# Optimization experiments

Measured on AMD Instinct MI355X. Metric: run time of the kernel, lower is better.

Reference implementation:

```python
import jax, jax.numpy as jnp
import numpy as np

B, S, E, D = 256, 256, 2, 128  # batch, seq_len, encoder_dim, decoder_dim


def setup_inputs() -> dict:
    key = jax.random.key(0)
    ks = jax.random.split(key, 9)
    u = lambda k, shape, n: jax.random.uniform(k, shape, jnp.float32, -1.0 / np.sqrt(n), 1.0 / np.sqrt(n))
    return {
        "out_encoder": jax.random.normal(ks[0], (B, S, E), jnp.float32),
        "W1_w": u(ks[1], (S, S), S),            # Linear(seq_len, seq_len)
        "W1_b": u(ks[2], (S,), S),
        "W2_w": u(ks[3], (S, 2 * S), 2 * S),    # Linear(2*seq_len, seq_len)
        "W2_b": u(ks[4], (S,), 2 * S),
        "W_ih": u(ks[5], (4 * D, E), D),        # LSTMCell input weights (i,f,g,o)
        "W_hh": u(ks[6], (4 * D, D), D),
        "b_ih": u(ks[7], (4 * D,), D),
        "b_hh": u(ks[8], (4 * D,), D),
    }


def reference(out_encoder, W1_w, W1_b, W2_w, W2_b, W_ih, W_hh, b_ih, b_hh):
    b, s, e = out_encoder.shape
    d = W_hh.shape[1]
    dt = out_encoder.dtype

    # W_2 term: encoder flattened to [B, 2S]; identical every step, hoist it.
    w2term = out_encoder.reshape(b, s * e) @ W2_w.T + W2_b          # [B, S]
    # W_1 applied to a row of S copies of h_d equals h_d * rowsum(W1) + b.
    w1sum = W1_w.sum(axis=1)                                        # [S]

    def attn(h):  # h: [B, D] -> context [B, E]
        hterm = h[:, :, None] * w1sum[None, None, :] + W1_b         # [B, D, S]
        en = jnp.tanh(w2term[:, None, :] + hterm)                   # [B, D, S]
        alpha = jax.nn.softmax(en, axis=-1).mean(axis=1)            # [B, S] (softmax over seq)
        return jnp.einsum('bs,bse->be', alpha, out_encoder)         # [B, E]

    def lstm_cell(x, h, c):
        gates = x @ W_ih.T + h @ W_hh.T + b_ih + b_hh               # [B, 4D]
        i, f, g, o = jnp.split(gates, 4, axis=-1)
        c = jax.nn.sigmoid(f) * c + jax.nn.sigmoid(i) * jnp.tanh(g)
        h = jax.nn.sigmoid(o) * jnp.tanh(c)
        return h, c

    h0 = jnp.zeros((b, d), dt)
    c0 = jnp.zeros((b, d), dt)

    def step(carry, _):
        h, c = carry
        x = attn(h)
        h, c = lstm_cell(x, h, c)
        return (h, c), h

    _, hs = jax.lax.scan(step, (h0, c0), None, length=s)
    return hs  # [S, B, D]: stacked decoder hidden states (original returns a list of h_t)
```

## Files before the change

### kernel.cpp

```cpp
#include <hip/hip_runtime.h>

#define NB 256
#define NS 256
#define NE 2
#define ND 128
#define NT 512
#define NN 16
#define RING 32
#define SLOT 144
#define SLOTH 160

typedef float vf4 __attribute__((ext_vector_type(4)));
typedef _Float16 f16x2 __attribute__((ext_vector_type(2)));

constexpr float L2E = 1.4426950408889634f;
constexpr float PI_F = 3.14159265358979323846f;

__device__ const float CT[16][16] = {
 {1,0,0,0,0,0,0,0,0,0,0,0,0,0,0,0},
 {0,1,0,0,0,0,0,0,0,0,0,0,0,0,0,0},
 {-1,0,2,0,0,0,0,0,0,0,0,0,0,0,0,0},
 {0,-3,0,4,0,0,0,0,0,0,0,0,0,0,0,0},
 {1,0,-8,0,8,0,0,0,0,0,0,0,0,0,0,0},
 {0,5,0,-20,0,16,0,0,0,0,0,0,0,0,0,0},
 {-1,0,18,0,-48,0,32,0,0,0,0,0,0,0,0,0},
 {0,-7,0,56,0,-112,0,64,0,0,0,0,0,0,0,0},
 {1,0,-32,0,160,0,-256,0,128,0,0,0,0,0,0,0},
 {0,9,0,-120,0,432,0,-576,0,256,0,0,0,0,0,0},
 {-1,0,50,0,-400,0,1120,0,-1280,0,512,0,0,0,0,0},
 {0,-11,0,220,0,-1232,0,2816,0,-2816,0,1024,0,0,0,0},
 {1,0,-72,0,840,0,-3584,0,6912,0,-6144,0,2048,0,0,0},
 {0,13,0,-364,0,2912,0,-9984,0,16640,0,-13312,0,4096,0,0},
 {-1,0,98,0,-1568,0,9408,0,-26880,0,39424,0,-28672,0,8192,0},
 {0,-15,0,560,0,-6048,0,28800,0,-70400,0,92160,0,-61440,0,16384}};

template <int C>
__device__ __forceinline__ float dppadd(float x) {
    return x + __builtin_bit_cast(float,
        __builtin_amdgcn_update_dpp(0, __builtin_bit_cast(int, x), C, 0xF, 0xF, true));
}
__device__ __forceinline__ float red_quad(float x) {
    x = dppadd<0xB1>(x); x = dppadd<0x4E>(x); return x;
}
__device__ __forceinline__ float red_oct(float x) {
    x = dppadd<0xB1>(x); x = dppadd<0x4E>(x); x = dppadd<0x141>(x); return x;
}
__device__ __forceinline__ float red_wave64(float x) {
    x = dppadd<0xB1>(x); x = dppadd<0x4E>(x); x = dppadd<0x141>(x);
    x = dppadd<0x140>(x); x = dppadd<0x142>(x); x = dppadd<0x143>(x); return x;
}
__device__ __forceinline__ float red_half32(float x) {
    x = dppadd<0xB1>(x); x = dppadd<0x4E>(x); x = dppadd<0x141>(x);
    x = dppadd<0x140>(x); x = dppadd<0x142>(x); return x;
}
__device__ __forceinline__ float red_grp16(float x) {
    x = dppadd<0x141>(x); x = dppadd<0x140>(x);
    x = dppadd<0x142>(x); x = dppadd<0x143>(x); return x;
}

__global__ __launch_bounds__(NT, 2)
void attn_lstm_decoder(const float* __restrict__ enc,
                       const float* __restrict__ W1w,
                       const float* __restrict__ W1b,
                       const float* __restrict__ W2w,
                       const float* __restrict__ W2b,
                       const float* __restrict__ Wih,
                       const float* __restrict__ Whh,
                       const float* __restrict__ bih,
                       const float* __restrict__ bhh,
                       float* __restrict__ out)
{
    const int b    = blockIdx.x;
    const int t    = threadIdx.x;
    const int wave = t >> 6;
    const int lane = t & 63;
    const int g    = t >> 2;
    const int q    = t & 3;
    const bool qb0 = q & 1;
    const bool qb1 = q & 2;
    const int half = lane >> 5;
    const int idx  = lane & 31;
    const int jnode = 2 * wave + half;

    __shared__ __align__(16) float    hist[RING * SLOT];
    __shared__ __align__(16) _Float16 hist16[RING * SLOTH];
    __shared__ __align__(16) float xwbuf[2][16];
    __shared__ float A2_l[NS];
    __shared__ float g2_l[NS];
    __shared__ float e0_l[NS];
    __shared__ float e1_l[NS];
    __shared__ float Ml[NN * NN];
    __shared__ float2 Pn[NN];
    __shared__ float2 Vl[NN];
    __shared__ float Pm0[NN], Pm1[NN];

    {
        float v = enc[b * (NS * NE) + t];
        if (t & 1) e1_l[t >> 1] = v; else e0_l[t >> 1] = v;
    }
    if (t < NN * NN) {
        const int mi = t >> 4, mj = t & 15;
        const float w = (mi == 0) ? (1.0f / NN) : (2.0f / NN);
        Ml[t] = w * __cosf((float)(mi * (2 * mj + 1)) * (PI_F / (2 * NN)));
    }
    __syncthreads();

    for (int r = 0; r < 32; ++r) {
        const int s = wave * 32 + r;
        float p = W1w[s * NS + lane]       + W1w[s * NS + lane + 64]
                + W1w[s * NS + lane + 128] + W1w[s * NS + lane + 192];
        p = red_wave64(p);
        if (lane == 63) g2_l[s] = p * (2.0f * L2E);
        float qq = 0.0f;
        #pragma unroll
        for (int kk = 0; kk < 8; ++kk) {
            const int c = lane + kk * 64;
            const float ev = (c & 1) ? e1_l[c >> 1] : e0_l[c >> 1];
            qq = fmaf(ev, W2w[s * (2 * NS) + c], qq);
        }
        qq = red_wave64(qq);
        if (lane == 63) A2_l[s] = (qq + W2b[s] + W1b[s]) * (2.0f * L2E);
    }
    __syncthreads();

    {
        const float y  = __cosf((float)(2 * jnode + 1) * (PI_F / (2 * NN)));
        const float C2 = -2.0f * L2E;
        float l = 0.0f, p0 = 0.0f, p1 = 0.0f;
        #pragma unroll
        for (int k = 0; k < 8; ++k) {
            const int s = k * 32 + idx;
            const float m1 = fmaf(y, g2_l[s], A2_l[s]);
            const float u  = __builtin_amdgcn_exp2f(m1);
            const float rc = __builtin_amdgcn_rcpf(u + 1.0f);
            const float e  = __builtin_amdgcn_exp2f(rc * C2);
            l += e;
            p0 = fmaf(e, e0_l[s], p0);
            p1 = fmaf(e, e1_l[s], p1);
        }
        l = red_half32(l); p0 = red_half32(p0); p1 = red_half32(p1);
        if ((lane & 31) == 31) {
            const float rl = __builtin_amdgcn_rcpf(l);
            Pn[jnode] = make_float2(p0 * rl, p1 * rl);
        }
    }
    __syncthreads();

    if (t < NN) {
        float v0 = 0.0f, v1 = 0.0f;
        #pragma unroll
        for (int j = 0; j < NN; ++j) {
            v0 = fmaf(Ml[t * NN + j], Pn[j].x, v0);
            v1 = fmaf(Ml[t * NN + j], Pn[j].y, v1);
        }
        Vl[t] = make_float2(v0 * (1.0f / ND), v1 * (1.0f / ND));
    }

    f16x2 wr16[4][16];
    float wi0_[4], wi1_[4], bb_[4];
    #pragma unroll
    for (int j = 0; j < 4; ++j) {
        const int r = g + 128 * j;
        const vf4* W4 = reinterpret_cast<const vf4*>(Whh + r * ND + q * 32);
        #pragma unroll
        for (int i = 0; i < 8; ++i) {
            const vf4 w = W4[i];
            wr16[j][2 * i + 0] = f16x2{(_Float16)w.x, (_Float16)w.y};
            wr16[j][2 * i + 1] = f16x2{(_Float16)w.z, (_Float16)w.w};
        }
        wi0_[j] = Wih[r * 2 + 0];
        wi1_[j] = Wih[r * 2 + 1];
        bb_[j]  = bih[r] + bhh[r];
    }

    if (t < ND) {
        hist[31 * SLOT + 36 * (t >> 5) + (t & 31)] = 0.0f;
        hist16[31 * SLOTH + 40 * (t >> 5) + (t & 31)] = (_Float16)0.0f;
    }
    float h_reg = 0.0f, c_reg = 0.0f;
    __syncthreads();

    if (t < NN) {
        float s0 = 0.0f, s1 = 0.0f;
        #pragma unroll
        for (int k = 0; k < NN; ++k) {
            s0 = fmaf(Vl[k].x, CT[k][t], s0);
            s1 = fmaf(Vl[k].y, CT[k][t], s1);
        }
        Pm0[t] = s0; Pm1[t] = s1;
    }
    __syncthreads();

    float Q0[4], Q1[4];
    #pragma unroll
    for (int i = 0; i < 4; ++i) { Q0[i] = Pm0[4 * i + q]; Q1[i] = Pm1[4 * i + q]; }

    auto phaseG = [&](float h, int pw) {
        const float h2 = h * h;
        const float h3 = h2 * h;
        const float h4 = h2 * h2;
        const float hq = qb1 ? (qb0 ? h3 : h2) : (qb0 ? h : 1.0f);
        float a0 = fmaf(Q0[3], h4, Q0[2]);
        a0 = fmaf(a0, h4, Q0[1]);
        a0 = fmaf(a0, h4, Q0[0]);
        float a1 = fmaf(Q1[3], h4, Q1[2]);
        a1 = fmaf(a1, h4, Q1[1]);
        a1 = fmaf(a1, h4, Q1[0]);
        a0 *= hq;
        a1 *= hq;
        a0 = red_quad(a0);  a1 = red_quad(a1);
        a0 = red_grp16(a0); a1 = red_grp16(a1);
        if (lane == 63) {
            xwbuf[pw][2 * wave + 0] = a0;
            xwbuf[pw][2 * wave + 1] = a1;
        }
    };

    phaseG(0.0f, 0);
    __syncthreads();

    for (int step = 0; step < NS; ++step) {
        const int pr = step & 1;
        const int rs = (step + RING - 1) & (RING - 1);
        const int ws = step & (RING - 1);

        float2 xv = *reinterpret_cast<const float2*>(&xwbuf[pr][2 * (lane & 7)]);
        const int4* hb = reinterpret_cast<const int4*>(&hist16[rs * SLOTH + q * 40]);
        int hw[16];
        #pragma unroll
        for (int i = 0; i < 4; ++i) {
            const int4 v = hb[i];
            hw[4 * i + 0] = v.x; hw[4 * i + 1] = v.y;
            hw[4 * i + 2] = v.z; hw[4 * i + 3] = v.w;
        }

        if ((step & 15) == 0 && step > 0) {
            const int sb  = (step - 16) & (RING - 1);
            const int k   = t >> 5;
            const int l32 = t & 31;
            const int w   = 4 * l32;
            const vf4 v = *reinterpret_cast<const vf4*>(
                &hist[(sb + k) * SLOT + 36 * (w >> 5) + (w & 31)]);
            *reinterpret_cast<vf4*>(
                &out[(size_t)(step - 16 + k) * (NB * ND) + b * ND + w]) = v;
        }

        float x0 = red_oct(xv.x);
        float x1 = red_oct(xv.y);

        float d0a = 0.f, d0b = 0.f, d1a = 0.f, d1b = 0.f;
        float d2a = 0.f, d2b = 0.f, d3a = 0.f, d3b = 0.f;
        #pragma unroll
        for (int i = 0; i < 8; ++i) {
            const f16x2 ha = __builtin_bit_cast(f16x2, hw[2 * i + 0]);
            const f16x2 hbv = __builtin_bit_cast(f16x2, hw[2 * i + 1]);
            d0a = __builtin_amdgcn_fdot2(wr16[0][2 * i + 0], ha,  d0a, false);
            d0b = __builtin_amdgcn_fdot2(wr16[0][2 * i + 1], hbv, d0b, false);
            d1a = __builtin_amdgcn_fdot2(wr16[1][2 * i + 0], ha,  d1a, false);
            d1b = __builtin_amdgcn_fdot2(wr16[1][2 * i + 1], hbv, d1b, false);
            d2a = __builtin_amdgcn_fdot2(wr16[2][2 * i + 0], ha,  d2a, false);
            d2b = __builtin_amdgcn_fdot2(wr16[2][2 * i + 1], hbv, d2b, false);
            d3a = __builtin_amdgcn_fdot2(wr16[3][2 * i + 0], ha,  d3a, false);
            d3b = __builtin_amdgcn_fdot2(wr16[3][2 * i + 1], hbv, d3b, false);
        }
        float d0 = d0a + d0b, d1 = d1a + d1b;
        float d2 = d2a + d2b, d3 = d3a + d3b;
        d0 = red_quad(d0);  d1 = red_quad(d1);
        d2 = red_quad(d2);  d3 = red_quad(d3);

        const float gi = d0 + fmaf(x0, wi0_[0], fmaf(x1, wi1_[0], bb_[0]));
        const float gf = d1 + fmaf(x0, wi0_[1], fmaf(x1, wi1_[1], bb_[1]));
        const float gg = d2 + fmaf(x0, wi0_[2], fmaf(x1, wi1_[2], bb_[2]));
        const float go = d3 + fmaf(x0, wi0_[3], fmaf(x1, wi1_[3], bb_[3]));

        const float si = __builtin_amdgcn_rcpf(1.0f + __builtin_amdgcn_exp2f(-L2E * gi));
        const float sf = __builtin_amdgcn_rcpf(1.0f + __builtin_amdgcn_exp2f(-L2E * gf));
        const float so = __builtin_amdgcn_rcpf(1.0f + __builtin_amdgcn_exp2f(-L2E * go));
        const float tg = 1.0f - 2.0f * __builtin_amdgcn_rcpf(__builtin_amdgcn_exp2f(2.0f * L2E * gg) + 1.0f);
        c_reg = sf * c_reg + si * tg;
        const float tc2 = 1.0f - 2.0f * __builtin_amdgcn_rcpf(__builtin_amdgcn_exp2f(2.0f * L2E * c_reg) + 1.0f);
        h_reg = so * tc2;

        if (q == 0) {
            hist[ws * SLOT + 36 * (g >> 5) + (g & 31)] = h_reg;
            hist16[ws * SLOTH + 40 * (g >> 5) + (g & 31)] = (_Float16)h_reg;
        }
        phaseG(h_reg, pr ^ 1);

        __syncthreads();
    }

    {
        const int k   = t >> 5;
        const int l32 = t & 31;
        const int w   = 4 * l32;
        const vf4 v = *reinterpret_cast<const vf4*>(
            &hist[(16 + k) * SLOT + 36 * (w >> 5) + (w & 31)]);
        *reinterpret_cast<vf4*>(
            &out[(size_t)(240 + k) * (NB * ND) + b * ND + w]) = v;
    }
}

extern "C" void kernel_launch(void* const* d_in, const int* in_sizes, int n_in,
                              void* d_out, int out_size, void* d_ws, size_t ws_size,
                              hipStream_t stream) {
    const float* enc = (const float*)d_in[0];
    const float* W1w = (const float*)d_in[1];
    const float* W1b = (const float*)d_in[2];
    const float* W2w = (const float*)d_in[3];
    const float* W2b = (const float*)d_in[4];
    const float* Wih = (const float*)d_in[5];
    const float* Whh = (const float*)d_in[6];
    const float* bih = (const float*)d_in[7];
    const float* bhh = (const float*)d_in[8];
    attn_lstm_decoder<<<NB, NT, 0, stream>>>(enc, W1w, W1b, W2w, W2b,
                                             Wih, Whh, bih, bhh, (float*)d_out);
}
```

Baseline: 303.7 us.

## Compute recurrent h·W_hh gates with MFMA instead of per-thread fdot2

Replaces the per-thread packed fp16 dot products for the recurrent gate matvec with 16x16x32 f16 MFMA tiles, where each wave owns 64 gate rows and the h vector is broadcast as the A operand. Only column 0 of each MFMA result is used. It is written to a new shared gate buffer and read back after an extra block barrier per step. This trades the shuffle reductions and the fdot2 chain for matrix-core work that is mostly wasted (15 of 16 columns), plus one more __syncthreads and an LDS round trip on the serial critical path.

```diff
diff --git a/kernel.cpp b/kernel.cpp
--- a/kernel.cpp
+++ b/kernel.cpp
@@ -11,7 +11,8 @@
 #define SLOTH 160
 
 typedef float vf4 __attribute__((ext_vector_type(4)));
-typedef _Float16 f16x2 __attribute__((ext_vector_type(2)));
+typedef _Float16 f16x8 __attribute__((ext_vector_type(8)));
+typedef float f32x4 __attribute__((ext_vector_type(4)));
 
 constexpr float L2E = 1.4426950408889634f;
 constexpr float PI_F = 3.14159265358979323846f;
@@ -78,6 +79,8 @@
     const int q    = t & 3;
     const bool qb0 = q & 1;
     const bool qb1 = q & 2;
+    const int grp  = lane >> 4;
+    const int nib  = lane & 15;
     const int half = lane >> 5;
     const int idx  = lane & 31;
     const int jnode = 2 * wave + half;
@@ -85,6 +88,7 @@
     __shared__ __align__(16) float    hist[RING * SLOT];
     __shared__ __align__(16) _Float16 hist16[RING * SLOTH];
     __shared__ __align__(16) float xwbuf[2][16];
+    __shared__ __align__(16) float gbuf[4 * ND];
     __shared__ float A2_l[NS];
     __shared__ float g2_l[NS];
     __shared__ float e0_l[NS];
@@ -156,18 +160,26 @@
         Vl[t] = make_float2(v0 * (1.0f / ND), v1 * (1.0f / ND));
     }
 
-    f16x2 wr16[4][16];
+    f16x8 wf[4][4];
     float wi0_[4], wi1_[4], bb_[4];
+    #pragma unroll
+    for (int rt = 0; rt < 4; ++rt) {
+        const int row = 64 * wave + 16 * rt + nib;
+        #pragma unroll
+        for (int kt = 0; kt < 4; ++kt) {
+            const vf4 wa = *reinterpret_cast<const vf4*>(Whh + row * ND + 32 * kt + 8 * grp);
+            const vf4 wb = *reinterpret_cast<const vf4*>(Whh + row * ND + 32 * kt + 8 * grp + 4);
+            f16x8 wv;
+            wv[0] = (_Float16)wa.x; wv[1] = (_Float16)wa.y;
+            wv[2] = (_Float16)wa.z; wv[3] = (_Float16)wa.w;
+            wv[4] = (_Float16)wb.x; wv[5] = (_Float16)wb.y;
+            wv[6] = (_Float16)wb.z; wv[7] = (_Float16)wb.w;
+            wf[rt][kt] = wv;
+        }
+    }
     #pragma unroll
     for (int j = 0; j < 4; ++j) {
         const int r = g + 128 * j;
-        const vf4* W4 = reinterpret_cast<const vf4*>(Whh + r * ND + q * 32);
-        #pragma unroll
-        for (int i = 0; i < 8; ++i) {
-            const vf4 w = W4[i];
-            wr16[j][2 * i + 0] = f16x2{(_Float16)w.x, (_Float16)w.y};
-            wr16[j][2 * i + 1] = f16x2{(_Float16)w.z, (_Float16)w.w};
-        }
         wi0_[j] = Wih[r * 2 + 0];
         wi1_[j] = Wih[r * 2 + 1];
         bb_[j]  = bih[r] + bhh[r];
@@ -224,15 +236,33 @@
         const int rs = (step + RING - 1) & (RING - 1);
         const int ws = step & (RING - 1);
 
+        f16x8 af[4];
+        const _Float16* hsl = &hist16[rs * SLOTH + 8 * grp];
+        #pragma unroll
+        for (int kt = 0; kt < 4; ++kt)
+            af[kt] = __builtin_bit_cast(f16x8,
+                *reinterpret_cast<const int4*>(hsl + 40 * kt));
+
+        f32x4 acc[4];
+        #pragma unroll
+        for (int rt = 0; rt < 4; ++rt) {
+            f32x4 a = {0.0f, 0.0f, 0.0f, 0.0f};
+            #pragma unroll
+            for (int kt = 0; kt < 4; ++kt)
+                a = __builtin_amdgcn_mfma_f32_16x16x32_f16(af[kt], wf[rt][kt], a, 0, 0, 0);
+            acc[rt] = a;
+        }
+        if (lane < 16) {
+            #pragma unroll
+            for (int rt = 0; rt < 4; ++rt) {
+                const int r = 64 * wave + 16 * rt + lane;
+                gbuf[((r & 127) << 2) | (r >> 7)] = acc[rt][0];
+            }
+        }
+        __syncthreads();
+
         float2 xv = *reinterpret_cast<const float2*>(&xwbuf[pr][2 * (lane & 7)]);
-        const int4* hb = reinterpret_cast<const int4*>(&hist16[rs * SLOTH + q * 40]);
-        int hw[16];
-        #pragma unroll
-        for (int i = 0; i < 4; ++i) {
-            const int4 v = hb[i];
-            hw[4 * i + 0] = v.x; hw[4 * i + 1] = v.y;
-            hw[4 * i + 2] = v.z; hw[4 * i + 3] = v.w;
-        }
+        const f32x4 gv = *reinterpret_cast<const f32x4*>(&gbuf[g << 2]);
 
         if ((step & 15) == 0 && step > 0) {
             const int sb  = (step - 16) & (RING - 1);
@@ -248,30 +278,10 @@
         float x0 = red_oct(xv.x);
         float x1 = red_oct(xv.y);
 
-        float d0a = 0.f, d0b = 0.f, d1a = 0.f, d1b = 0.f;
-        float d2a = 0.f, d2b = 0.f, d3a = 0.f, d3b = 0.f;
-        #pragma unroll
-        for (int i = 0; i < 8; ++i) {
-            const f16x2 ha = __builtin_bit_cast(f16x2, hw[2 * i + 0]);
-            const f16x2 hbv = __builtin_bit_cast(f16x2, hw[2 * i + 1]);
-            d0a = __builtin_amdgcn_fdot2(wr16[0][2 * i + 0], ha,  d0a, false);
-            d0b = __builtin_amdgcn_fdot2(wr16[0][2 * i + 1], hbv, d0b, false);
-            d1a = __builtin_amdgcn_fdot2(wr16[1][2 * i + 0], ha,  d1a, false);
-            d1b = __builtin_amdgcn_fdot2(wr16[1][2 * i + 1], hbv, d1b, false);
-            d2a = __builtin_amdgcn_fdot2(wr16[2][2 * i + 0], ha,  d2a, false);
-            d2b = __builtin_amdgcn_fdot2(wr16[2][2 * i + 1], hbv, d2b, false);
-            d3a = __builtin_amdgcn_fdot2(wr16[3][2 * i + 0], ha,  d3a, false);
-            d3b = __builtin_amdgcn_fdot2(wr16[3][2 * i + 1], hbv, d3b, false);
-        }
-        float d0 = d0a + d0b, d1 = d1a + d1b;
-        float d2 = d2a + d2b, d3 = d3a + d3b;
-        d0 = red_quad(d0);  d1 = red_quad(d1);
-        d2 = red_quad(d2);  d3 = red_quad(d3);
-
-        const float gi = d0 + fmaf(x0, wi0_[0], fmaf(x1, wi1_[0], bb_[0]));
-        const float gf = d1 + fmaf(x0, wi0_[1], fmaf(x1, wi1_[1], bb_[1]));
-        const float gg = d2 + fmaf(x0, wi0_[2], fmaf(x1, wi1_[2], bb_[2]));
-        const float go = d3 + fmaf(x0, wi0_[3], fmaf(x1, wi1_[3], bb_[3]));
+        const float gi = gv[0] + fmaf(x0, wi0_[0], fmaf(x1, wi1_[0], bb_[0]));
+        const float gf = gv[1] + fmaf(x0, wi0_[1], fmaf(x1, wi1_[1], bb_[1]));
+        const float gg = gv[2] + fmaf(x0, wi0_[2], fmaf(x1, wi1_[2], bb_[2]));
+        const float go = gv[3] + fmaf(x0, wi0_[3], fmaf(x1, wi1_[3], bb_[3]));
 
         const float si = __builtin_amdgcn_rcpf(1.0f + __builtin_amdgcn_exp2f(-L2E * gi));
         const float sf = __builtin_amdgcn_rcpf(1.0f + __builtin_amdgcn_exp2f(-L2E * gf));
```

Result: no change. 303.7 us (-0.0%).
